# Optimization experiments

Hardware: AMD Instinct MI355X
Metric: run time of the kernel (lower is better)

The kernel has to match this reference:

```python
import jax, jax.numpy as jnp
import numpy as np

N = 8192
F_IN = 256
F_OUT = 128


def setup_inputs() -> dict:
    key = jax.random.key(0)
    k1, k2, k3, k4 = jax.random.split(key, 4)
    input = jax.random.normal(k1, (N, F_IN), dtype=jnp.float32)
    adj = jax.random.uniform(k2, (N, N), dtype=jnp.float32)
    stdv = 1.0 / np.sqrt(F_OUT)
    weight = jax.random.uniform(k3, (F_IN, F_OUT), dtype=jnp.float32, minval=-stdv, maxval=stdv)
    bias = jax.random.uniform(k4, (F_OUT,), dtype=jnp.float32, minval=-stdv, maxval=stdv)
    return {"input": input, "adj": adj, "weight": weight, "bias": bias}


def reference(input, adj, weight, bias):
    # adj = adj + I  (self loops)
    n = adj.shape[0]
    adj = adj + jnp.eye(n, dtype=adj.dtype)
    # degree inverse, with NaN (from nan entries) zeroed like temp[temp != temp] = 0
    deg_inv = 1.0 / jnp.sum(adj, axis=1)  # [N]
    deg_inv = jnp.where(jnp.isnan(deg_inv), 0.0, deg_inv)
    # D @ adj is just a row-scale; avoid materializing diag(deg_inv)
    adj_norm = deg_inv[:, None] * adj  # [N, N]
    support = input @ weight           # [N, F_out]
    output = adj_norm @ support        # [N, F_out]
    return output + bias
```

## Files before the change

### kernel.cpp

```cpp
#include <hip/hip_runtime.h>
#include <stdint.h>


#define NROW 8192
#define FIN 256
#define FOUT 128
#define KSPLIT 4
#define KCH (NROW / KSPLIT)

typedef __attribute__((ext_vector_type(8))) short bf16x8;
typedef __attribute__((ext_vector_type(4))) float f32x4;

static __device__ __forceinline__ unsigned short f2bf(float x) {
  unsigned u = __builtin_bit_cast(unsigned, x);
  u = (u + 0x7FFFu + ((u >> 16) & 1u)) >> 16;
  return (unsigned short)u;
}

__global__ __launch_bounds__(256) void k_support(
    const float* __restrict__ input, const float* __restrict__ weight,
    float* __restrict__ support, unsigned short* __restrict__ supportT) {
  __shared__ __align__(16) float in_lds[16 * FIN];
  __shared__ __align__(16) float tr_lds[16 * (FOUT + 4)];
  const int t = threadIdx.x;
  const int rbase = blockIdx.x * 16;
  const float* src = input + (size_t)rbase * FIN;
#pragma unroll
  for (int c = 0; c < 4; ++c) {
    const int idx = c * 1024 + t * 4;
    *(float4*)&in_lds[idx] = *(const float4*)&src[idx];
  }
  __syncthreads();
  const int j = t & 127;
  const int rg = t >> 7;
  float acc[8] = {0.f, 0.f, 0.f, 0.f, 0.f, 0.f, 0.f, 0.f};
  for (int f = 0; f < FIN; f += 4) {
    const float w0 = weight[(f + 0) * FOUT + j];
    const float w1 = weight[(f + 1) * FOUT + j];
    const float w2 = weight[(f + 2) * FOUT + j];
    const float w3 = weight[(f + 3) * FOUT + j];
#pragma unroll
    for (int r = 0; r < 8; ++r) {
      const float4 iv = *(const float4*)&in_lds[(rg * 8 + r) * FIN + f];
      acc[r] += iv.x * w0 + iv.y * w1 + iv.z * w2 + iv.w * w3;
    }
  }
#pragma unroll
  for (int r = 0; r < 8; ++r) {
    const int row = rbase + rg * 8 + r;
    support[(size_t)row * FOUT + j] = acc[r];
    tr_lds[(rg * 8 + r) * (FOUT + 4) + j] = acc[r];
  }
  __syncthreads();
  const int r = t & 15, g = t >> 4;
#pragma unroll
  for (int jj = 0; jj < 8; ++jj) {
    const int jc = jj * 16 + g;
    const float v = tr_lds[r * (FOUT + 4) + jc];
    supportT[(size_t)jc * NROW + rbase + r] = f2bf(v);
  }
}

__global__ __launch_bounds__(512, 4) void k_spmm(
    const float* __restrict__ adj, const unsigned short* __restrict__ supportT,
    float* __restrict__ partial, float* __restrict__ degp) {
  __shared__ __align__(16) unsigned char bT[FOUT * 64];
  const int t = threadIdx.x;
  const int w = t >> 6, l = t & 63;
  const int rb = blockIdx.x >> 2;
  const int ks = blockIdx.x & 3;
  const int rbase = rb * 64;
  const int kbase = ks * KCH;
  const int rg = w >> 1, cg = w & 1;
  const int l15 = l & 15, kg = l >> 4;

  const int sn = t >> 2;
  const int su = t & 3;
  const int sup = su ^ ((sn >> 1) & 3);
  const uint4* sgp = (const uint4*)(supportT + (size_t)sn * NROW + kbase + su * 8);
  uint4* slp = (uint4*)(bT + sn * 64 + sup * 16);

  const int arow = rbase + rg * 16 + l15;
  const float* aptr = adj + (size_t)arow * NROW + kbase + kg * 8;

  f32x4 acc[4] = {};
  float rs = 0.f;

  for (int s = 0; s < KCH / 32; ++s) {
    const float4 a0 = *(const float4*)(aptr + s * 32);
    const float4 a1 = *(const float4*)(aptr + s * 32 + 4);
    __syncthreads();
    *slp = sgp[s * 4];
    __syncthreads();
    rs += ((a0.x + a0.y) + (a0.z + a0.w)) + ((a1.x + a1.y) + (a1.z + a1.w));
    bf16x8 af;
    af[0] = (short)f2bf(a0.x); af[1] = (short)f2bf(a0.y);
    af[2] = (short)f2bf(a0.z); af[3] = (short)f2bf(a0.w);
    af[4] = (short)f2bf(a1.x); af[5] = (short)f2bf(a1.y);
    af[6] = (short)f2bf(a1.z); af[7] = (short)f2bf(a1.w);
#pragma unroll
    for (int tt = 0; tt < 4; ++tt) {
      const int n = cg * 64 + tt * 16 + l15;
      const int up = kg ^ ((n >> 1) & 3);
      const bf16x8 bfv = *(const bf16x8*)(bT + n * 64 + up * 16);
      acc[tt] = __builtin_amdgcn_mfma_f32_16x16x32_bf16(af, bfv, acc[tt], 0, 0, 0);
    }
  }

  rs += __shfl_xor(rs, 16, 64);
  rs += __shfl_xor(rs, 32, 64);
  if (cg == 0 && l < 16)
    degp[ks * NROW + rbase + rg * 16 + l] = rs;

  float* pout = partial + (size_t)ks * NROW * FOUT;
  const int prow = rbase + rg * 16 + kg * 4;
  const int pcol = cg * 64 + l15;
#pragma unroll
  for (int tt = 0; tt < 4; ++tt)
#pragma unroll
    for (int q = 0; q < 4; ++q)
      pout[(size_t)(prow + q) * FOUT + pcol + tt * 16] = acc[tt][q];
}

__global__ __launch_bounds__(256) void k_final(
    const float* __restrict__ partial, const float* __restrict__ degp,
    const float* __restrict__ support, const float* __restrict__ bias,
    float* __restrict__ out) {
  const int idx = blockIdx.x * 256 + threadIdx.x;
  const int e = idx * 4;
  const int i = e >> 7;
  const int j = e & 127;
  float d = 1.0f + degp[i] + degp[NROW + i] + degp[2 * NROW + i] + degp[3 * NROW + i];
  float dinv = 1.0f / d;
  if (dinv != dinv) dinv = 0.f;
  const float4 p0 = *(const float4*)&partial[e];
  const float4 p1 = *(const float4*)&partial[(1u << 20) + e];
  const float4 p2 = *(const float4*)&partial[(2u << 20) + e];
  const float4 p3 = *(const float4*)&partial[(3u << 20) + e];
  const float4 sv = *(const float4*)&support[e];
  const float4 bv = *(const float4*)&bias[j];
  float4 o;
  o.x = (p0.x + p1.x + p2.x + p3.x + sv.x) * dinv + bv.x;
  o.y = (p0.y + p1.y + p2.y + p3.y + sv.y) * dinv + bv.y;
  o.z = (p0.z + p1.z + p2.z + p3.z + sv.z) * dinv + bv.z;
  o.w = (p0.w + p1.w + p2.w + p3.w + sv.w) * dinv + bv.w;
  *(float4*)&out[e] = o;
}

extern "C" void kernel_launch(void* const* d_in, const int* in_sizes, int n_in,
                              void* d_out, int out_size, void* d_ws, size_t ws_size,
                              hipStream_t stream) {
  const float* input  = (const float*)d_in[0];
  const float* adj    = (const float*)d_in[1];
  const float* weight = (const float*)d_in[2];
  const float* bias   = (const float*)d_in[3];
  float* out = (float*)d_out;
  float* ws = (float*)d_ws;
  float* support = ws;
  float* partial = ws + (1u << 20);
  float* degp    = ws + (5u << 20);
  unsigned short* supportT = (unsigned short*)(degp + NROW * KSPLIT);

  k_support<<<NROW / 16, 256, 0, stream>>>(input, weight, support, supportT);
  k_spmm<<<(NROW / 64) * KSPLIT, 512, 0, stream>>>(adj, supportT, partial, degp);
  k_final<<<(NROW * FOUT / 4) / 256, 256, 0, stream>>>(partial, degp, support, bias, out);
}
```

Before: 131.1 us.

## Double-buffer supportT tiles in LDS with a wider K-step in spmm

Widens each k_spmm iteration from 32 to 128 K columns and double-buffers the bf16 supportT tile in LDS. The global loads for the next tile are issued before the MFMA work on the current one, which cuts barriers from two per 32 columns to one per 128. The adj fp32-to-bf16 conversion moves from manual integer rounding to the hardware v_cvt_pk_bf16_f32 instruction. LDS per block rises to 64KB and register pressure grows (eight float4 adj loads plus prefetch registers), which may lower occupancy under the 4-blocks launch bound.

```diff
diff --git a/kernel.cpp b/kernel.cpp
--- a/kernel.cpp
+++ b/kernel.cpp
@@ -64,7 +64,7 @@
 __global__ __launch_bounds__(512, 4) void k_spmm(
     const float* __restrict__ adj, const unsigned short* __restrict__ supportT,
     float* __restrict__ partial, float* __restrict__ degp) {
-  __shared__ __align__(16) unsigned char bT[FOUT * 64];
+  __shared__ __align__(16) unsigned char bT[2][FOUT * 256];
   const int t = threadIdx.x;
   const int w = t >> 6, l = t & 63;
   const int rb = blockIdx.x >> 2;
@@ -75,10 +75,11 @@
   const int l15 = l & 15, kg = l >> 4;
 
   const int sn = t >> 2;
-  const int su = t & 3;
-  const int sup = su ^ ((sn >> 1) & 3);
-  const uint4* sgp = (const uint4*)(supportT + (size_t)sn * NROW + kbase + su * 8);
-  uint4* slp = (uint4*)(bT + sn * 64 + sup * 16);
+  const int ub = (t & 3) * 4;
+  const unsigned short* sgp = supportT + (size_t)sn * NROW + kbase;
+  int wo[4];
+#pragma unroll
+  for (int j = 0; j < 4; ++j) wo[j] = sn * 256 + (((ub + j) ^ (sn & 15)) << 4);
 
   const int arow = rbase + rg * 16 + l15;
   const float* aptr = adj + (size_t)arow * NROW + kbase + kg * 8;
@@ -86,25 +87,53 @@
   f32x4 acc[4] = {};
   float rs = 0.f;
 
-  for (int s = 0; s < KCH / 32; ++s) {
-    const float4 a0 = *(const float4*)(aptr + s * 32);
-    const float4 a1 = *(const float4*)(aptr + s * 32 + 4);
+  {
+    uint4 bv0[4];
+#pragma unroll
+    for (int j = 0; j < 4; ++j) bv0[j] = *(const uint4*)(sgp + (ub + j) * 8);
+#pragma unroll
+    for (int j = 0; j < 4; ++j) *(uint4*)&bT[0][wo[j]] = bv0[j];
+  }
+  __syncthreads();
+
+  for (int s = 0; s < 16; ++s) {
+    const unsigned char* rbuf = bT[s & 1];
+    uint4 bv[4];
+    if (s < 15) {
+#pragma unroll
+      for (int j = 0; j < 4; ++j)
+        bv[j] = *(const uint4*)(sgp + (s + 1) * 128 + (ub + j) * 8);
+    }
+    float4 av[8];
+#pragma unroll
+    for (int i = 0; i < 4; ++i) {
+      av[2 * i]     = *(const float4*)(aptr + s * 128 + i * 32);
+      av[2 * i + 1] = *(const float4*)(aptr + s * 128 + i * 32 + 4);
+    }
+#pragma unroll
+    for (int i = 0; i < 4; ++i) {
+      const float4 a0 = av[2 * i], a1 = av[2 * i + 1];
+      rs += ((a0.x + a0.y) + (a0.z + a0.w)) + ((a1.x + a1.y) + (a1.z + a1.w));
+      int4 pk;
+      asm("v_cvt_pk_bf16_f32 %0, %1, %2" : "=v"(pk.x) : "v"(a0.x), "v"(a0.y));
+      asm("v_cvt_pk_bf16_f32 %0, %1, %2" : "=v"(pk.y) : "v"(a0.z), "v"(a0.w));
+      asm("v_cvt_pk_bf16_f32 %0, %1, %2" : "=v"(pk.z) : "v"(a1.x), "v"(a1.y));
+      asm("v_cvt_pk_bf16_f32 %0, %1, %2" : "=v"(pk.w) : "v"(a1.z), "v"(a1.w));
+      const bf16x8 af = __builtin_bit_cast(bf16x8, pk);
+      const int swz = ((i * 4 + kg) ^ l15) << 4;
+#pragma unroll
+      for (int tt = 0; tt < 4; ++tt) {
+        const int n = cg * 64 + tt * 16 + l15;
+        const bf16x8 bfv = *(const bf16x8*)(rbuf + n * 256 + swz);
+        acc[tt] = __builtin_amdgcn_mfma_f32_16x16x32_bf16(af, bfv, acc[tt], 0, 0, 0);
+      }
+    }
+    if (s < 15) {
+      unsigned char* wbuf = bT[(s + 1) & 1];
+#pragma unroll
+      for (int j = 0; j < 4; ++j) *(uint4*)&wbuf[wo[j]] = bv[j];
+    }
     __syncthreads();
-    *slp = sgp[s * 4];
-    __syncthreads();
-    rs += ((a0.x + a0.y) + (a0.z + a0.w)) + ((a1.x + a1.y) + (a1.z + a1.w));
-    bf16x8 af;
-    af[0] = (short)f2bf(a0.x); af[1] = (short)f2bf(a0.y);
-    af[2] = (short)f2bf(a0.z); af[3] = (short)f2bf(a0.w);
-    af[4] = (short)f2bf(a1.x); af[5] = (short)f2bf(a1.y);
-    af[6] = (short)f2bf(a1.z); af[7] = (short)f2bf(a1.w);
-#pragma unroll
-    for (int tt = 0; tt < 4; ++tt) {
-      const int n = cg * 64 + tt * 16 + l15;
-      const int up = kg ^ ((n >> 1) & 3);
-      const bf16x8 bfv = *(const bf16x8*)(bT + n * 64 + up * 16);
-      acc[tt] = __builtin_amdgcn_mfma_f32_16x16x32_bf16(af, bfv, acc[tt], 0, 0, 0);
-    }
   }
 
   rs += __shfl_xor(rs, 16, 64);
```

New measurement: 144.2 us. 9.9% more time.

## Fuse epilogue into spmm, drop K-split, add double-buffered LDS pipeline with 32x32 MFMA

Applied to the files above, without the earlier changes.

Removes the K-split partial-sum scheme and the separate final kernel. Each block now covers 32 full rows and applies degree normalization, the support self-loop and the bias in its epilogue. The main loop stages adj (converted to bf16) and supportT through double-buffered, XOR-swizzled LDS, with register prefetch two stages ahead and 32x32x16 MFMAs. The two K-half waves are reduced through LDS. This removes the partial buffer round-trip and a launch, but the grid shrinks to 256 blocks, which may reduce memory-level parallelism on the streaming adj read.

```diff
diff --git a/kernel.cpp b/kernel.cpp
--- a/kernel.cpp
+++ b/kernel.cpp
@@ -5,11 +5,11 @@
 #define NROW 8192
 #define FIN 256
 #define FOUT 128
-#define KSPLIT 4
-#define KCH (NROW / KSPLIT)
+#define SK 64
+#define NST (NROW / SK)
 
 typedef __attribute__((ext_vector_type(8))) short bf16x8;
-typedef __attribute__((ext_vector_type(4))) float f32x4;
+typedef __attribute__((ext_vector_type(16))) float f32x16;
 
 static __device__ __forceinline__ unsigned short f2bf(float x) {
   unsigned u = __builtin_bit_cast(unsigned, x);
@@ -56,95 +56,115 @@
 #pragma unroll
   for (int jj = 0; jj < 8; ++jj) {
     const int jc = jj * 16 + g;
-    const float v = tr_lds[r * (FOUT + 4) + jc];
-    supportT[(size_t)jc * NROW + rbase + r] = f2bf(v);
+    supportT[(size_t)jc * NROW + rbase + r] = f2bf(tr_lds[r * (FOUT + 4) + jc]);
   }
 }
 
-__global__ __launch_bounds__(512, 4) void k_spmm(
+__global__ __launch_bounds__(512, 2) void k_spmm(
     const float* __restrict__ adj, const unsigned short* __restrict__ supportT,
-    float* __restrict__ partial, float* __restrict__ degp) {
-  __shared__ __align__(16) unsigned char bT[FOUT * 64];
+    const float* __restrict__ support, const float* __restrict__ bias,
+    float* __restrict__ out) {
+  __shared__ __align__(16) unsigned char LDS[41088];
   const int t = threadIdx.x;
-  const int w = t >> 6, l = t & 63;
-  const int rb = blockIdx.x >> 2;
-  const int ks = blockIdx.x & 3;
-  const int rbase = rb * 64;
-  const int kbase = ks * KCH;
-  const int rg = w >> 1, cg = w & 1;
-  const int l15 = l & 15, kg = l >> 4;
+  const int l = t & 63, w = t >> 6;
+  const int cg = w >> 1, kw = w & 1;
+  const int l31 = l & 31, kg = l >> 5;
+  const int rbase = blockIdx.x * 32;
 
-  const int sn = t >> 2;
-  const int su = t & 3;
-  const int sup = su ^ ((sn >> 1) & 3);
-  const uint4* sgp = (const uint4*)(supportT + (size_t)sn * NROW + kbase + su * 8);
-  uint4* slp = (uint4*)(bT + sn * 64 + sup * 16);
+  const int sr = t >> 4, sc = t & 15;
+  const float* aG = adj + (size_t)(rbase + sr) * NROW + sc * 4;
+  const int aL = sr * 128 + ((((sc >> 1)) ^ (sr & 7)) << 4) + (sc & 1) * 8;
+  const int bcol = t >> 2, bj = t & 3;
+  const unsigned short* bG = supportT + (size_t)bcol * NROW + bj * 16;
+  const int bL0 = 8192 + bcol * 128 + (((bj * 2) ^ (bcol & 7)) << 4);
+  const int bL1 = 8192 + bcol * 128 + (((bj * 2 + 1) ^ (bcol & 7)) << 4);
 
-  const int arow = rbase + rg * 16 + l15;
-  const float* aptr = adj + (size_t)arow * NROW + kbase + kg * 8;
+  const int u0 = kw * 4 + kg;
+  const int aF0 = l31 * 128 + ((u0 ^ (l31 & 7)) << 4);
+  const int aF1 = l31 * 128 + (((u0 + 2) ^ (l31 & 7)) << 4);
+  const int colg = cg * 32 + l31;
+  const int bF0 = 8192 + colg * 128 + ((u0 ^ (colg & 7)) << 4);
+  const int bF1 = 8192 + colg * 128 + (((u0 + 2) ^ (colg & 7)) << 4);
 
-  f32x4 acc[4] = {};
+  struct Stage { float4 a; uint4 b0, b1; };
+  Stage S0, S1;
   float rs = 0.f;
+  f32x16 acc;
+#pragma unroll
+  for (int q = 0; q < 16; ++q) acc[q] = 0.f;
 
-  for (int s = 0; s < KCH / 32; ++s) {
-    const float4 a0 = *(const float4*)(aptr + s * 32);
-    const float4 a1 = *(const float4*)(aptr + s * 32 + 4);
-    __syncthreads();
-    *slp = sgp[s * 4];
-    __syncthreads();
-    rs += ((a0.x + a0.y) + (a0.z + a0.w)) + ((a1.x + a1.y) + (a1.z + a1.w));
-    bf16x8 af;
-    af[0] = (short)f2bf(a0.x); af[1] = (short)f2bf(a0.y);
-    af[2] = (short)f2bf(a0.z); af[3] = (short)f2bf(a0.w);
-    af[4] = (short)f2bf(a1.x); af[5] = (short)f2bf(a1.y);
-    af[6] = (short)f2bf(a1.z); af[7] = (short)f2bf(a1.w);
+  auto load_stage = [&](Stage& S, int s) {
+    S.a = *(const float4*)(aG + s * SK);
+    S.b0 = *(const uint4*)(bG + (size_t)s * SK);
+    S.b1 = *(const uint4*)(bG + (size_t)s * SK + 8);
+  };
+  auto store_stage = [&](const Stage& S, int buf) {
+    rs += (S.a.x + S.a.y) + (S.a.z + S.a.w);
+    uint2 p;
+    asm("v_cvt_pk_bf16_f32 %0, %1, %2" : "=v"(p.x) : "v"(S.a.x), "v"(S.a.y));
+    asm("v_cvt_pk_bf16_f32 %0, %1, %2" : "=v"(p.y) : "v"(S.a.z), "v"(S.a.w));
+    *(uint2*)(LDS + buf * 4096 + aL) = p;
+    *(uint4*)(LDS + buf * 16384 + bL0) = S.b0;
+    *(uint4*)(LDS + buf * 16384 + bL1) = S.b1;
+  };
+  auto compute = [&](int buf) {
+    const bf16x8 a0 = *(const bf16x8*)(LDS + buf * 4096 + aF0);
+    const bf16x8 b0 = *(const bf16x8*)(LDS + buf * 16384 + bF0);
+    const bf16x8 a1 = *(const bf16x8*)(LDS + buf * 4096 + aF1);
+    const bf16x8 b1 = *(const bf16x8*)(LDS + buf * 16384 + bF1);
+    acc = __builtin_amdgcn_mfma_f32_32x32x16_bf16(a0, b0, acc, 0, 0, 0);
+    acc = __builtin_amdgcn_mfma_f32_32x32x16_bf16(a1, b1, acc, 0, 0, 0);
+  };
+
+  load_stage(S0, 0);
+  load_stage(S1, 1);
+  store_stage(S0, 0);
+  load_stage(S0, 2);
+  asm volatile("s_waitcnt lgkmcnt(0)" ::: "memory");
+  __builtin_amdgcn_s_barrier();
+
+  for (int s = 0; s < NST; ++s) {
+    const int buf = s & 1;
+    compute(buf);
+    if (s + 1 < NST) {
+      if (buf == 0) {
+        store_stage(S1, 1);
+        if (s + 3 < NST) load_stage(S1, s + 3);
+      } else {
+        store_stage(S0, 0);
+        if (s + 3 < NST) load_stage(S0, s + 3);
+      }
+    }
+    asm volatile("s_waitcnt lgkmcnt(0)" ::: "memory");
+    __builtin_amdgcn_s_barrier();
+  }
+
+  rs += __shfl_xor(rs, 1, 64);
+  rs += __shfl_xor(rs, 2, 64);
+  rs += __shfl_xor(rs, 4, 64);
+  rs += __shfl_xor(rs, 8, 64);
+  if ((l & 15) == 0) *(float*)(LDS + 40960 + (w * 4 + (l >> 4)) * 4) = rs;
+
+  float* mb = (float*)(LDS + cg * 4096);
+  if (kw) {
 #pragma unroll
-    for (int tt = 0; tt < 4; ++tt) {
-      const int n = cg * 64 + tt * 16 + l15;
-      const int up = kg ^ ((n >> 1) & 3);
-      const bf16x8 bfv = *(const bf16x8*)(bT + n * 64 + up * 16);
-      acc[tt] = __builtin_amdgcn_mfma_f32_16x16x32_bf16(af, bfv, acc[tt], 0, 0, 0);
+    for (int q = 0; q < 16; ++q) mb[q * 64 + l] = acc[q];
+  }
+  asm volatile("s_waitcnt lgkmcnt(0)" ::: "memory");
+  __builtin_amdgcn_s_barrier();
+
+  if (!kw) {
+#pragma unroll
+    for (int q = 0; q < 16; ++q) {
+      const int row = (q & 3) + 8 * (q >> 2) + 4 * kg;
+      const float v = acc[q] + mb[q * 64 + l];
+      const float deg = 1.f + *(const float*)(LDS + 40960 + row * 4);
+      float dinv = 1.f / deg;
+      if (dinv != dinv) dinv = 0.f;
+      const size_t o = (size_t)(rbase + row) * FOUT + colg;
+      out[o] = (v + support[o]) * dinv + bias[colg];
     }
   }
-
-  rs += __shfl_xor(rs, 16, 64);
-  rs += __shfl_xor(rs, 32, 64);
-  if (cg == 0 && l < 16)
-    degp[ks * NROW + rbase + rg * 16 + l] = rs;
-
-  float* pout = partial + (size_t)ks * NROW * FOUT;
-  const int prow = rbase + rg * 16 + kg * 4;
-  const int pcol = cg * 64 + l15;
-#pragma unroll
-  for (int tt = 0; tt < 4; ++tt)
-#pragma unroll
-    for (int q = 0; q < 4; ++q)
-      pout[(size_t)(prow + q) * FOUT + pcol + tt * 16] = acc[tt][q];
-}
-
-__global__ __launch_bounds__(256) void k_final(
-    const float* __restrict__ partial, const float* __restrict__ degp,
-    const float* __restrict__ support, const float* __restrict__ bias,
-    float* __restrict__ out) {
-  const int idx = blockIdx.x * 256 + threadIdx.x;
-  const int e = idx * 4;
-  const int i = e >> 7;
-  const int j = e & 127;
-  float d = 1.0f + degp[i] + degp[NROW + i] + degp[2 * NROW + i] + degp[3 * NROW + i];
-  float dinv = 1.0f / d;
-  if (dinv != dinv) dinv = 0.f;
-  const float4 p0 = *(const float4*)&partial[e];
-  const float4 p1 = *(const float4*)&partial[(1u << 20) + e];
-  const float4 p2 = *(const float4*)&partial[(2u << 20) + e];
-  const float4 p3 = *(const float4*)&partial[(3u << 20) + e];
-  const float4 sv = *(const float4*)&support[e];
-  const float4 bv = *(const float4*)&bias[j];
-  float4 o;
-  o.x = (p0.x + p1.x + p2.x + p3.x + sv.x) * dinv + bv.x;
-  o.y = (p0.y + p1.y + p2.y + p3.y + sv.y) * dinv + bv.y;
-  o.z = (p0.z + p1.z + p2.z + p3.z + sv.z) * dinv + bv.z;
-  o.w = (p0.w + p1.w + p2.w + p3.w + sv.w) * dinv + bv.w;
-  *(float4*)&out[e] = o;
 }
 
 extern "C" void kernel_launch(void* const* d_in, const int* in_sizes, int n_in,
@@ -157,11 +177,8 @@
   float* out = (float*)d_out;
   float* ws = (float*)d_ws;
   float* support = ws;
-  float* partial = ws + (1u << 20);
-  float* degp    = ws + (5u << 20);
-  unsigned short* supportT = (unsigned short*)(degp + NROW * KSPLIT);
+  unsigned short* supportT = (unsigned short*)(ws + (size_t)NROW * FOUT);
 
   k_support<<<NROW / 16, 256, 0, stream>>>(input, weight, support, supportT);
-  k_spmm<<<(NROW / 64) * KSPLIT, 512, 0, stream>>>(adj, supportT, partial, degp);
-  k_final<<<(NROW * FOUT / 4) / 256, 256, 0, stream>>>(partial, degp, support, bias, out);
+  k_spmm<<<NROW / 32, 512, 0, stream>>>(adj, supportT, support, bias, out);
 }
```

Measured after the change: 151.3 us. 15.4% more time.
